# Optimization experiments

Measured on AMD Instinct MI355X. Metric: run time of the kernel, lower is better.

The kernel has to match this reference:

```python
import jax, jax.numpy as jnp
import numpy as np

V, K, H, B = 50000, 50, 300, 512
C_WEIGHTS = 0.0005
C_TOPICS = 5e-06
BN_EPS = 1e-5


def _bn(x, g, b, m, v):
    # eval-mode BatchNorm1d with running stats
    return (x - m) * jax.lax.rsqrt(v + BN_EPS) * g + b


def setup_inputs() -> dict:
    key = jax.random.key(0)
    ks = jax.random.split(key, 16)
    s = 0.02
    inp = {
        "bows": jax.random.uniform(ks[0], (B, V), jnp.float32),
        "normalized_bows": jax.random.uniform(ks[1], (B, V), jnp.float32),
        "labels": jax.random.normal(ks[2], (B,), jnp.float32),
        # encoder q_theta: Linear(V,H) -> relu -> BN -> Linear(H,H) -> relu -> BN
        "W1": jax.random.normal(ks[3], (H, V), jnp.float32) * s,
        "b1": jnp.zeros((H,), jnp.float32),
        "W2": jax.random.normal(ks[4], (H, H), jnp.float32) * s,
        "b2": jnp.zeros((H,), jnp.float32),
        "bn1_g": jnp.ones((H,), jnp.float32),
        "bn1_b": jnp.zeros((H,), jnp.float32),
        "bn1_m": jnp.zeros((H,), jnp.float32),
        "bn1_v": jnp.ones((H,), jnp.float32),
        "bn2_g": jnp.ones((H,), jnp.float32),
        "bn2_b": jnp.zeros((H,), jnp.float32),
        "bn2_m": jnp.zeros((H,), jnp.float32),
        "bn2_v": jnp.ones((H,), jnp.float32),
        "muW": jax.random.normal(ks[5], (K, H), jnp.float32) * s,
        "mub": jnp.zeros((K,), jnp.float32),
        "lsW": jax.random.normal(ks[6], (K, H), jnp.float32) * s,
        "lsb": jnp.zeros((K,), jnp.float32),
        "logit_betas": jax.random.normal(ks[7], (V, K), jnp.float32),
        "gammas": jax.random.normal(ks[8], (V, K), jnp.float32),
        "base_rates": jax.random.normal(ks[9], (V,), jnp.float32),
        "bow_w": jax.random.normal(ks[10], (V,), jnp.float32) * s,
        "bow_b": jnp.zeros((), jnp.float32),
        "topic_w": jax.random.normal(ks[11], (K,), jnp.float32) * s,
        "topic_b": jnp.zeros((), jnp.float32),
    }
    return inp


def reference(bows, normalized_bows, labels, W1, b1, W2, b2,
              bn1_g, bn1_b, bn1_m, bn1_v, bn2_g, bn2_b, bn2_m, bn2_v,
              muW, mub, lsW, lsb, logit_betas, gammas, base_rates,
              bow_w, bow_b, topic_w, topic_b):
    # ---- encode (eval mode: reparameterize returns mu) ----
    h = _bn(jax.nn.relu(normalized_bows @ W1.T + b1), bn1_g, bn1_b, bn1_m, bn1_v)
    h = _bn(jax.nn.relu(h @ W2.T + b2), bn2_g, bn2_b, bn2_m, bn2_v)
    mu = h @ muW.T + mub                       # [B, K]
    logsigma = h @ lsW.T + lsb                 # [B, K]
    kld_theta = -0.5 * jnp.mean(jnp.sum(1.0 + logsigma - mu ** 2 - jnp.exp(logsigma), axis=-1))
    theta = jax.nn.softmax(mu, axis=-1)        # [B, K]

    # ---- decode + reconstruction loss ----
    logits = theta @ logit_betas.T + base_rates          # [B, V]
    preds = jnp.log(jax.nn.softmax(logits, axis=-1) + 1e-06)
    recon_loss = -jnp.mean(jnp.sum(preds * bows, axis=1))

    # ---- other_loss: L1 on base_rates ----
    other_loss = C_WEIGHTS * jnp.sum(jnp.abs(base_rates))

    # ---- predict_labels (hstm-all), reordered contraction: (bows @ scaled_beta) * theta
    scaled_beta = logit_betas * gammas                   # [V, K]
    het_term = jnp.sum((normalized_bows @ scaled_beta) * theta, axis=1)  # == (bows * (theta @ scaled_beta.T)).sum(1)
    expected_pred = het_term + (normalized_bows @ bow_w + bow_b) + (theta @ topic_w + topic_b)

    other_loss = other_loss + jnp.mean((expected_pred - labels) ** 2)
    other_loss = other_loss + C_TOPICS * jnp.sum(jnp.abs(gammas))
    other_loss = other_loss + C_WEIGHTS * jnp.linalg.norm(bow_w)

    return recon_loss, other_loss, kld_theta
```

## Files before the change

kernel.cpp:

```cpp
#include <hip/hip_runtime.h>
#include <hip/hip_bf16.h>
#include <math.h>


#define B_  512
#define V_  50000
#define VP  50016
#define K_  50
#define H_  300
#define KP  64
#define NW  384
#define NSTEP 1563
#define NCVT 7327
#define NSB  782
#define NACV 12504

typedef __attribute__((ext_vector_type(8))) short short8;
typedef __attribute__((ext_vector_type(4))) float f32x4;

static __device__ __forceinline__ short bf16s(float f) {
  unsigned int u = __builtin_bit_cast(unsigned int, f);
  u += 0x7fffu + ((u >> 16) & 1u);
  return (short)(u >> 16);
}

static __device__ __forceinline__ unsigned int pkbf(float lo, float hi) {
  __hip_bfloat162 t = __float22bfloat162_rn(float2{lo, hi});
  unsigned int u; __builtin_memcpy(&u, &t, 4); return u;
}

static __device__ __forceinline__ short8 to_bf8(float4 a, float4 b) {
  unsigned int u[4];
  u[0] = pkbf(a.x, a.y); u[1] = pkbf(a.z, a.w);
  u[2] = pkbf(b.x, b.y); u[3] = pkbf(b.z, b.w);
  short8 r; __builtin_memcpy(&r, u, 16); return r;
}

__global__ __launch_bounds__(256) void k_prep(
    const float* __restrict__ W1,
    const float* __restrict__ beta, const float* __restrict__ gamma,
    const float* __restrict__ br,   const float* __restrict__ bw,
    const float* __restrict__ nb,
    short* __restrict__ Wcatb, short* __restrict__ betab,
    short* __restrict__ nbb,
    float* __restrict__ pg, float* __restrict__ pbr, float* __restrict__ pbw2)
{
  __shared__ short sbt[64 * 52];
  __shared__ short bbt[64 * 52];
  __shared__ float redA[4];
  const int tid = threadIdx.x;
  const short8 z8 = {0, 0, 0, 0, 0, 0, 0, 0};

  if (blockIdx.x < NCVT) {
    const int idx = blockIdx.x * 256 + tid;
    if (idx >= NSTEP * 300 * 4) return;
    const int st = idx / 1200;
    const int rem = idx - st * 1200;
    const int n = rem >> 2, kq = rem & 3;
    const int kbase = st * 32 + kq * 8;
    short8 o = z8;
    if (kbase + 8 <= V_) {
      const float4* p = (const float4*)(W1 + (size_t)n * V_ + kbase);
      o = to_bf8(p[0], p[1]);
    }
    *(short8*)(Wcatb + (size_t)st * 12288 + n * 32 + kq * 8) = o;
    return;
  }

  if (blockIdx.x >= NCVT + NSB) {
    const int idx = (blockIdx.x - (NCVT + NSB)) * 256 + tid;
    const int st = idx >> 11;
    const int r  = (idx >> 2) & 511;
    const int kq = idx & 3;
    const int kbase = st * 32 + kq * 8;
    short8 o = z8;
    if (kbase + 8 <= V_) {
      const float4* p = (const float4*)(nb + (size_t)r * V_ + kbase);
      o = to_bf8(p[0], p[1]);
    }
    *(short8*)(nbb + (size_t)st * 16384 + r * 32 + kq * 8) = o;
    return;
  }

  const int blk = blockIdx.x - NCVT;
  const int v0 = blk * 64;
  const int nvalid = (V_ - v0 < 64) ? (V_ - v0) : 64;
  const int nwrite = (VP - v0 < 64) ? (VP - v0) : 64;

  const int nf4 = (nvalid * 50) / 4;
  const float4* bsrc = (const float4*)(beta  + (size_t)v0 * 50);
  const float4* gsrc = (const float4*)(gamma + (size_t)v0 * 50);
  float gabs = 0.f;
  for (int f = tid; f < nf4; f += 256) {
    float4 bv = bsrc[f];
    float4 gv = gsrc[f];
    float be[4] = {bv.x, bv.y, bv.z, bv.w};
    float ge[4] = {gv.x, gv.y, gv.z, gv.w};
    #pragma unroll
    for (int e = 0; e < 4; ++e) {
      int idx = f * 4 + e;
      int j = idx / 50, k = idx - j * 50;
      gabs += fabsf(ge[e]);
      bbt[j * 52 + k] = bf16s(be[e]);
      sbt[j * 52 + k] = bf16s(be[e] * ge[e]);
    }
  }
  #pragma unroll
  for (int off = 1; off < 64; off <<= 1) gabs += __shfl_xor(gabs, off, 64);
  if ((tid & 63) == 0) redA[tid >> 6] = gabs;
  if (tid < 64) {
    float s1 = 0.f, s2 = 0.f;
    if (tid < nvalid) {
      s1 = fabsf(br[v0 + tid]);
      float w = bw[v0 + tid]; s2 = w * w;
    }
    #pragma unroll
    for (int off = 1; off < 64; off <<= 1) {
      s1 += __shfl_xor(s1, off, 64);
      s2 += __shfl_xor(s2, off, 64);
    }
    if (tid == 0) { pbr[blk] = s1; pbw2[blk] = s2; }
  }
  __syncthreads();
  if (tid == 0) pg[blk] = redA[0] + redA[1] + redA[2] + redA[3];

  const int j = tid & 63;
  const int q = tid >> 6;
  #pragma unroll
  for (int p = 0; p < 21; ++p) {
    const int kk = p * 4 + q;
    if (j < nwrite) {
      short val = 0;
      if (j < nvalid) {
        if (kk >= 20 && kk < 70)      val = sbt[j * 52 + (kk - 20)];
        else if (kk == 70)            val = bf16s(bw[v0 + j]);
      }
      Wcatb[(size_t)(blk * 2 + (j >> 5)) * 12288 + (300 + kk) * 32 + (j & 31)] = val;
    }
  }
  if (j < nvalid) {
    __attribute__((aligned(16))) short tmp[16];
    #pragma unroll
    for (int t = 0; t < 16; ++t) {
      int k = q * 16 + t;
      tmp[t] = (k < K_) ? bbt[j * 52 + k] : (short)0;
    }
    short8* dst = (short8*)(betab + (size_t)(v0 + j) * 64 + q * 16);
    dst[0] = *(const short8*)&tmp[0];
    dst[1] = *(const short8*)&tmp[8];
  }
}

__global__ __launch_bounds__(256, 3) void k_bg(
    const short* __restrict__ Ab, const short* __restrict__ Bb,
    float* __restrict__ part, int sps)
{
  const int t = blockIdx.x;
  const int s = t / 12;
  const int r = t % 12;
  const int bni = r % 3, bmi = r / 3;
  const int lane = threadIdx.x & 63, wv = threadIdx.x >> 6;
  const int l15 = lane & 15, quad = lane >> 4;
  const int m0 = bmi * 128 + (wv & 1) * 64;
  const int n0 = bni * 128 + (wv >> 1) * 64;
  int st0 = s * sps, st1 = st0 + sps;
  if (st0 > NSTEP) st0 = NSTEP;
  if (st1 > NSTEP) st1 = NSTEP;
  const int nst = st1 - st0;

  const short8* pa = (const short8*)Ab + (size_t)st0 * 2048 + (m0 + l15) * 4 + quad;
  const short8* pb = (const short8*)Bb + (size_t)st0 * 1536 + (n0 + l15) * 4 + quad;

  f32x4 acc[4][4];
  #pragma unroll
  for (int i = 0; i < 4; ++i)
    #pragma unroll
    for (int jj = 0; jj < 4; ++jj) acc[i][jj] = f32x4{0.f, 0.f, 0.f, 0.f};

  short8 A0[4], A1[4], B0[4], B1[4];

  auto ld = [&](short8 (&Af)[4], short8 (&Bf)[4]) {
    #pragma unroll
    for (int i = 0; i < 4; ++i) Af[i] = pa[i * 64];
    #pragma unroll
    for (int jj = 0; jj < 4; ++jj) Bf[jj] = pb[jj * 64];
    pa += 2048; pb += 1536;
  };
  auto comp = [&](short8 (&Af)[4], short8 (&Bf)[4]) {
    #pragma unroll
    for (int i = 0; i < 4; ++i)
      #pragma unroll
      for (int jj = 0; jj < 4; ++jj)
        acc[i][jj] = __builtin_amdgcn_mfma_f32_16x16x32_bf16(Af[i], Bf[jj], acc[i][jj], 0, 0, 0);
  };

  if (nst > 0) {
    ld(A0, B0);
    int k = 0;
    for (; k + 2 <= nst; k += 2) {
      ld(A1, B1);
      comp(A0, B0);
      if (k + 2 < nst) ld(A0, B0);
      comp(A1, B1);
    }
    if (k < nst) comp(A0, B0);
  }

  float* op = part + (size_t)s * (B_ * NW);
  #pragma unroll
  for (int i = 0; i < 4; ++i)
    #pragma unroll
    for (int jj = 0; jj < 4; ++jj)
      #pragma unroll
      for (int rr = 0; rr < 4; ++rr)
        op[(size_t)(m0 + 16 * i + quad * 4 + rr) * NW + (n0 + 16 * jj + l15)] = acc[i][jj][rr];
}

__global__ __launch_bounds__(320) void k_mlp(
    const float* __restrict__ part, int S,
    const float* __restrict__ b1,
    const float* __restrict__ g1, const float* __restrict__ bb1,
    const float* __restrict__ m1, const float* __restrict__ v1,
    const float* __restrict__ W2, const float* __restrict__ b2,
    const float* __restrict__ g2, const float* __restrict__ bb2,
    const float* __restrict__ m2, const float* __restrict__ v2,
    const float* __restrict__ muW, const float* __restrict__ mub,
    const float* __restrict__ lsW, const float* __restrict__ lsb,
    short* __restrict__ thetab, float* __restrict__ thetaf,
    float* __restrict__ hetmat, float* __restrict__ kldp)
{
  __shared__ __attribute__((aligned(16))) float h1s[H_];
  __shared__ __attribute__((aligned(16))) float h2s[H_];
  const int b = blockIdx.x;
  const int tid = threadIdx.x;
  const float* pb = part + (size_t)b * NW;

  if (tid < H_) {
    float s0 = 0.f, s1 = 0.f, s2 = 0.f, s3 = 0.f;
    int i = 0;
    for (; i + 4 <= S; i += 4) {
      s0 += pb[(size_t)(i + 0) * (B_ * NW) + tid];
      s1 += pb[(size_t)(i + 1) * (B_ * NW) + tid];
      s2 += pb[(size_t)(i + 2) * (B_ * NW) + tid];
      s3 += pb[(size_t)(i + 3) * (B_ * NW) + tid];
    }
    for (; i < S; ++i) s0 += pb[(size_t)i * (B_ * NW) + tid];
    float s = (s0 + s1) + (s2 + s3);
    float x = fmaxf(s + b1[tid], 0.f);
    h1s[tid] = (x - m1[tid]) * rsqrtf(v1[tid] + 1e-5f) * g1[tid] + bb1[tid];
  }
  if (tid < 51) {
    float s0 = 0.f, s1 = 0.f;
    int i = 0;
    for (; i + 2 <= S; i += 2) {
      s0 += pb[(size_t)(i + 0) * (B_ * NW) + 320 + tid];
      s1 += pb[(size_t)(i + 1) * (B_ * NW) + 320 + tid];
    }
    for (; i < S; ++i) s0 += pb[(size_t)i * (B_ * NW) + 320 + tid];
    hetmat[(size_t)b * KP + tid] = s0 + s1;
  }
  __syncthreads();
  if (tid < H_) {
    const float4* wr = (const float4*)(W2 + (size_t)tid * H_);
    const float4* hr = (const float4*)h1s;
    float acc = 0.f;
    for (int q = 0; q < H_ / 4; ++q) {
      float4 w = wr[q], h = hr[q];
      acc += w.x * h.x + w.y * h.y + w.z * h.z + w.w * h.w;
    }
    float x = fmaxf(acc + b2[tid], 0.f);
    h2s[tid] = (x - m2[tid]) * rsqrtf(v2[tid] + 1e-5f) * g2[tid] + bb2[tid];
  }
  __syncthreads();
  if (tid < 64) {
    float mu = 0.f, ls = 0.f;
    if (tid < K_) {
      const float4* mr = (const float4*)(muW + (size_t)tid * H_);
      const float4* lr = (const float4*)(lsW + (size_t)tid * H_);
      const float4* hr = (const float4*)h2s;
      for (int q = 0; q < H_ / 4; ++q) {
        float4 h = hr[q], a = mr[q], c = lr[q];
        mu += a.x * h.x + a.y * h.y + a.z * h.z + a.w * h.w;
        ls += c.x * h.x + c.y * h.y + c.z * h.z + c.w * h.w;
      }
      mu += mub[tid]; ls += lsb[tid];
    }
    float term = (tid < K_) ? (1.f + ls - mu * mu - __expf(ls)) : 0.f;
    float ts = term;
    #pragma unroll
    for (int off = 1; off < 64; off <<= 1) ts += __shfl_xor(ts, off, 64);
    if (tid == 0) kldp[b] = ts;
    float mv = (tid < K_) ? mu : -INFINITY;
    #pragma unroll
    for (int off = 1; off < 64; off <<= 1) mv = fmaxf(mv, __shfl_xor(mv, off, 64));
    float e = (tid < K_) ? __expf(mu - mv) : 0.f;
    float se = e;
    #pragma unroll
    for (int off = 1; off < 64; off <<= 1) se += __shfl_xor(se, off, 64);
    float tv = (tid < K_) ? (e / se) : 0.f;
    thetaf[(size_t)b * KP + tid] = tv;
    thetab[(size_t)b * KP + tid] = bf16s(tv);
  }
}

__global__ __launch_bounds__(256, 2) void k_c1(
    const short* __restrict__ thetab, const short* __restrict__ betab,
    const float* __restrict__ br, float* __restrict__ c1p)
{
  const int blk = blockIdx.x;
  const int bm = blk & 7, vs = blk >> 3;
  const int lane = threadIdx.x & 63, wv = threadIdx.x >> 6;
  const int l15 = lane & 15, quad = lane >> 4;
  const int b0 = bm * 64 + wv * 16;
  const short8* arow = (const short8*)(thetab + (size_t)(b0 + l15) * KP);
  const short8 a0 = arow[quad], a1 = arow[4 + quad];
  int t0 = vs * 33, t1 = t0 + 33; if (t1 > 3125) t1 = 3125;
  float p0 = 0.f, p1 = 0.f, p2 = 0.f, p3 = 0.f;
  auto body = [&](int tt) {
    const int v0 = tt * 16;
    const short8* brow = (const short8*)(betab + (size_t)(v0 + l15) * KP);
    short8 q0 = brow[quad], q1 = brow[4 + quad];
    f32x4 acc = {0.f, 0.f, 0.f, 0.f};
    acc = __builtin_amdgcn_mfma_f32_16x16x32_bf16(a0, q0, acc, 0, 0, 0);
    acc = __builtin_amdgcn_mfma_f32_16x16x32_bf16(a1, q1, acc, 0, 0, 0);
    const float brv = br[v0 + l15];
    p0 += __expf(acc[0] + brv);
    p1 += __expf(acc[1] + brv);
    p2 += __expf(acc[2] + brv);
    p3 += __expf(acc[3] + brv);
  };
  int tt = t0;
  for (; tt + 2 <= t1; tt += 2) { body(tt); body(tt + 1); }
  if (tt < t1) body(tt);
  #pragma unroll
  for (int off = 1; off < 16; off <<= 1) {
    p0 += __shfl_xor(p0, off, 16);
    p1 += __shfl_xor(p1, off, 16);
    p2 += __shfl_xor(p2, off, 16);
    p3 += __shfl_xor(p3, off, 16);
  }
  if (l15 == 0) {
    float* dst = c1p + (size_t)vs * B_ + b0 + quad * 4;
    dst[0] = p0; dst[1] = p1; dst[2] = p2; dst[3] = p3;
  }
}

static __device__ __forceinline__ float blockred512(float x, float* red) {
  #pragma unroll
  for (int off = 1; off < 64; off <<= 1) x += __shfl_xor(x, off, 64);
  if ((threadIdx.x & 63) == 0) red[threadIdx.x >> 6] = x;
  __syncthreads();
  float r = 0.f;
  if (threadIdx.x == 0)
    for (int i = 0; i < 8; ++i) r += red[i];
  __syncthreads();
  return r;
}

__global__ __launch_bounds__(512) void k_d1(
    const float* __restrict__ c1p, const float* __restrict__ kldp,
    const float* __restrict__ pg, const float* __restrict__ pbr,
    const float* __restrict__ pbw2,
    const float* __restrict__ hetmat, const float* __restrict__ thetaf,
    const float* __restrict__ labels, const float* __restrict__ topic_w,
    const float* __restrict__ topic_b, const float* __restrict__ bow_b,
    float* __restrict__ lseb, float* __restrict__ out)
{
  __shared__ float red[8];
  const int b = threadIdx.x;
  float se = 0.f;
  for (int i = 0; i < 96; ++i) se += c1p[(size_t)i * B_ + b];
  lseb[b] = __logf(se);
  float het = 0.f, tpc = 0.f;
  #pragma unroll
  for (int k = 0; k < K_; ++k) {
    float th = thetaf[(size_t)b * KP + k];
    het += th * hetmat[(size_t)b * KP + k];
    tpc += th * topic_w[k];
  }
  float ep = het + hetmat[(size_t)b * KP + 50] + bow_b[0] + tpc + topic_b[0];
  float d = ep - labels[b];
  float mse  = blockred512(d * d, red);
  float kl   = blockred512(kldp[b], red);
  float sg = 0.f, sr = 0.f, sw = 0.f;
  for (int i = b; i < NSB; i += 512) { sg += pg[i]; sr += pbr[i]; sw += pbw2[i]; }
  sg = blockred512(sg, red);
  sr = blockred512(sr, red);
  sw = blockred512(sw, red);
  if (b == 0) {
    out[1] = 0.0005f * sr + mse / (float)B_ + 5e-6f * sg + 0.0005f * sqrtf(sw);
    out[2] = -0.5f * kl / (float)B_;
  }
}

__global__ __launch_bounds__(256, 2) void k_c2(
    const short* __restrict__ thetab, const short* __restrict__ betab,
    const float* __restrict__ br, const float* __restrict__ lseb,
    const float* __restrict__ bows, float* __restrict__ c2p)
{
  __shared__ float red[4];
  const int blk = blockIdx.x;
  const int bm = blk & 7, vs = blk >> 3;
  const int lane = threadIdx.x & 63, wv = threadIdx.x >> 6;
  const int l15 = lane & 15, quad = lane >> 4;
  const int b0 = bm * 64 + wv * 16;
  const short8* arow = (const short8*)(thetab + (size_t)(b0 + l15) * KP);
  const short8 a0 = arow[quad], a1 = arow[4 + quad];
  float lse4[4]; const float* bro[4];
  #pragma unroll
  for (int rr = 0; rr < 4; ++rr) {
    lse4[rr] = lseb[b0 + quad * 4 + rr];
    bro[rr] = bows + (size_t)(b0 + quad * 4 + rr) * V_;
  }
  int t0 = vs * 33, t1 = t0 + 33; if (t1 > 3125) t1 = 3125;
  float p = 0.f;
  auto body = [&](int tt) {
    const int v0 = tt * 16;
    const int v = v0 + l15;
    const short8* brow = (const short8*)(betab + (size_t)v * KP);
    short8 q0 = brow[quad], q1 = brow[4 + quad];
    f32x4 acc = {0.f, 0.f, 0.f, 0.f};
    acc = __builtin_amdgcn_mfma_f32_16x16x32_bf16(a0, q0, acc, 0, 0, 0);
    acc = __builtin_amdgcn_mfma_f32_16x16x32_bf16(a1, q1, acc, 0, 0, 0);
    const float brv = br[v];
    #pragma unroll
    for (int rr = 0; rr < 4; ++rr) {
      float l = acc[rr] + brv - lse4[rr];
      float pr = __logf(__expf(l) + 1e-6f);
      p += pr * bro[rr][v];
    }
  };
  int tt = t0;
  for (; tt + 2 <= t1; tt += 2) { body(tt); body(tt + 1); }
  if (tt < t1) body(tt);
  #pragma unroll
  for (int off = 1; off < 64; off <<= 1) p += __shfl_xor(p, off, 64);
  if (lane == 0) red[wv] = p;
  __syncthreads();
  if (threadIdx.x == 0) c2p[blk] = red[0] + red[1] + red[2] + red[3];
}

__global__ __launch_bounds__(256) void k_d2(
    const float* __restrict__ c2p, float* __restrict__ out)
{
  __shared__ float red[4];
  float s = 0.f;
  for (int i = threadIdx.x; i < 768; i += 256) s += c2p[i];
  #pragma unroll
  for (int off = 1; off < 64; off <<= 1) s += __shfl_xor(s, off, 64);
  if ((threadIdx.x & 63) == 0) red[threadIdx.x >> 6] = s;
  __syncthreads();
  if (threadIdx.x == 0)
    out[0] = -(red[0] + red[1] + red[2] + red[3]) / (float)B_;
}

extern "C" void kernel_launch(void* const* d_in, const int* in_sizes, int n_in,
                              void* d_out, int out_size, void* d_ws, size_t ws_size,
                              hipStream_t stream)
{
  const float* bows    = (const float*)d_in[0];
  const float* nb      = (const float*)d_in[1];
  const float* labels  = (const float*)d_in[2];
  const float* W1      = (const float*)d_in[3];
  const float* b1      = (const float*)d_in[4];
  const float* W2      = (const float*)d_in[5];
  const float* b2      = (const float*)d_in[6];
  const float* bn1_g   = (const float*)d_in[7];
  const float* bn1_b   = (const float*)d_in[8];
  const float* bn1_m   = (const float*)d_in[9];
  const float* bn1_v   = (const float*)d_in[10];
  const float* bn2_g   = (const float*)d_in[11];
  const float* bn2_b   = (const float*)d_in[12];
  const float* bn2_m   = (const float*)d_in[13];
  const float* bn2_v   = (const float*)d_in[14];
  const float* muW     = (const float*)d_in[15];
  const float* mub     = (const float*)d_in[16];
  const float* lsW     = (const float*)d_in[17];
  const float* lsb     = (const float*)d_in[18];
  const float* beta    = (const float*)d_in[19];
  const float* gamma   = (const float*)d_in[20];
  const float* brates  = (const float*)d_in[21];
  const float* bow_w   = (const float*)d_in[22];
  const float* bow_b   = (const float*)d_in[23];
  const float* topic_w = (const float*)d_in[24];
  const float* topic_b = (const float*)d_in[25];
  float* out = (float*)d_out;

  char* ws = (char*)d_ws;
  size_t off = 0;
  auto take = [&](size_t bytes) { void* p = ws + off; off = (off + bytes + 255) & ~(size_t)255; return p; };

  short* Wcatb   = (short*)take((size_t)NSTEP * 12288 * 2);
  short* nbb     = (short*)take((size_t)NSTEP * 16384 * 2);
  short* betab   = (short*)take((size_t)V_ * 64 * 2);
  short* thetab  = (short*)take((size_t)B_ * KP * 2);
  float* thetaf  = (float*)take((size_t)B_ * KP * 4);
  float* hetmat  = (float*)take((size_t)B_ * KP * 4);
  float* kldp    = (float*)take((size_t)B_ * 4);
  float* c1p     = (float*)take((size_t)96 * B_ * 4);
  float* c2p     = (float*)take((size_t)768 * 4);
  float* lse_    = (float*)take((size_t)B_ * 4);
  float* pg      = (float*)take((size_t)NSB * 4);
  float* pbr     = (float*)take((size_t)NSB * 4);
  float* pbw2    = (float*)take((size_t)NSB * 4);
  float* part1   = (float*)(ws + off);
  size_t remain = (ws_size > off) ? (ws_size - off) : 0;
  int S = (int)(remain / ((size_t)B_ * NW * 4));
  if (S > 64) S = 64;
  if (S < 1)  S = 1;
  const int sps = (NSTEP + S - 1) / S;

  k_prep<<<NCVT + NSB + NACV, 256, 0, stream>>>(
      W1, beta, gamma, brates, bow_w, nb, Wcatb, betab, nbb, pg, pbr, pbw2);
  k_bg  <<<12 * S, 256, 0, stream>>>(nbb, Wcatb, part1, sps);
  k_mlp <<<B_, 320, 0, stream>>>(part1, S, b1, bn1_g, bn1_b, bn1_m, bn1_v,
                                 W2, b2, bn2_g, bn2_b, bn2_m, bn2_v,
                                 muW, mub, lsW, lsb, thetab, thetaf, hetmat, kldp);
  k_c1  <<<8 * 96, 256, 0, stream>>>(thetab, betab, brates, c1p);
  k_d1  <<<1, 512, 0, stream>>>(c1p, kldp, pg, pbr, pbw2, hetmat, thetaf,
                                labels, topic_w, topic_b, bow_b, lse_, out);
  k_c2  <<<8 * 96, 256, 0, stream>>>(thetab, betab, brates, lse_, bows, c2p);
  k_d2  <<<1, 256, 0, stream>>>(c2p, out);
}
```

Baseline: 478.8 us.

## Tile bf16 conversion of W1 and normalized_bows through LDS for coalesced access

```diff
diff --git a/kernel.cpp b/kernel.cpp
--- a/kernel.cpp
+++ b/kernel.cpp
@@ -11,9 +11,11 @@
 #define KP  64
 #define NW  384
 #define NSTEP 1563
-#define NCVT 7327
 #define NSB  782
-#define NACV 12504
+#define TS   8
+#define NT_ST 196
+#define NB_W1T (5*NT_ST)
+#define NB_NBT (8*NT_ST)
 
 typedef __attribute__((ext_vector_type(8))) short short8;
 typedef __attribute__((ext_vector_type(4))) float f32x4;
@@ -27,13 +29,6 @@
 static __device__ __forceinline__ unsigned int pkbf(float lo, float hi) {
   __hip_bfloat162 t = __float22bfloat162_rn(float2{lo, hi});
   unsigned int u; __builtin_memcpy(&u, &t, 4); return u;
-}
-
-static __device__ __forceinline__ short8 to_bf8(float4 a, float4 b) {
-  unsigned int u[4];
-  u[0] = pkbf(a.x, a.y); u[1] = pkbf(a.z, a.w);
-  u[2] = pkbf(b.x, b.y); u[3] = pkbf(b.z, b.w);
-  short8 r; __builtin_memcpy(&r, u, 16); return r;
 }
 
 __global__ __launch_bounds__(256) void k_prep(
@@ -45,44 +40,60 @@
     short* __restrict__ nbb,
     float* __restrict__ pg, float* __restrict__ pbr, float* __restrict__ pbw2)
 {
-  __shared__ short sbt[64 * 52];
-  __shared__ short bbt[64 * 52];
-  __shared__ float redA[4];
+  __shared__ __attribute__((aligned(16))) short lds[16384];
   const int tid = threadIdx.x;
-  const short8 z8 = {0, 0, 0, 0, 0, 0, 0, 0};
-
-  if (blockIdx.x < NCVT) {
-    const int idx = blockIdx.x * 256 + tid;
-    if (idx >= NSTEP * 300 * 4) return;
-    const int st = idx / 1200;
-    const int rem = idx - st * 1200;
-    const int n = rem >> 2, kq = rem & 3;
-    const int kbase = st * 32 + kq * 8;
-    short8 o = z8;
-    if (kbase + 8 <= V_) {
-      const float4* p = (const float4*)(W1 + (size_t)n * V_ + kbase);
-      o = to_bf8(p[0], p[1]);
-    }
-    *(short8*)(Wcatb + (size_t)st * 12288 + n * 32 + kq * 8) = o;
+
+  if (blockIdx.x < NB_W1T || blockIdx.x >= NB_W1T + NSB) {
+    const float* src; short* dst; int r0, nrows, frame, blk;
+    if (blockIdx.x < NB_W1T) {
+      blk = blockIdx.x; src = W1; dst = Wcatb; frame = 12288;
+      const int band = blk / NT_ST;
+      r0 = band * 64; nrows = (band == 4) ? 44 : 64;
+    } else {
+      blk = blockIdx.x - (NB_W1T + NSB); src = nb; dst = nbb; frame = 16384;
+      const int band = blk / NT_ST;
+      r0 = band * 64; nrows = 64;
+    }
+    const int stile = blk % NT_ST;
+    const int s0 = stile * TS;
+    int ns = NSTEP - s0; if (ns > TS) ns = TS;
+
+    const int row = tid >> 2, p = tid & 3;
+    if (row < nrows) {
+      const float4* rp = (const float4*)(src + (size_t)(r0 + row) * V_) + (size_t)s0 * 8;
+      const int c4lim = 12500 - s0 * 8;
+      auto doj = [&](int j) {
+        const int f4 = p + 4 * j;
+        float4 v = {0.f, 0.f, 0.f, 0.f};
+        if (f4 < c4lim) v = rp[f4];
+        unsigned int u0 = pkbf(v.x, v.y), u1 = pkbf(v.z, v.w);
+        unsigned long long uu = ((unsigned long long)u1 << 32) | (unsigned long long)u0;
+        *(unsigned long long*)((char*)lds + ((f4 >> 3) * 4096 + row * 64 + (f4 & 7) * 8)) = uu;
+      };
+      if (ns == TS) {
+        #pragma unroll
+        for (int jj = 0; jj < 8; ++jj) doj(jj);
+        #pragma unroll
+        for (int jj = 8; jj < 16; ++jj) doj(jj);
+      } else {
+        for (int j = 0; j < 2 * ns; ++j) doj(j);
+      }
+    }
+    __syncthreads();
+    for (int stl = 0; stl < ns; ++stl) {
+      short* db = dst + (size_t)(s0 + stl) * frame + r0 * 32;
+      const short8* sb = (const short8*)((char*)lds + stl * 4096);
+      for (int w = tid; w < nrows * 4; w += 256)
+        *(short8*)(db + w * 8) = sb[w];
+    }
     return;
   }
 
-  if (blockIdx.x >= NCVT + NSB) {
-    const int idx = (blockIdx.x - (NCVT + NSB)) * 256 + tid;
-    const int st = idx >> 11;
-    const int r  = (idx >> 2) & 511;
-    const int kq = idx & 3;
-    const int kbase = st * 32 + kq * 8;
-    short8 o = z8;
-    if (kbase + 8 <= V_) {
-      const float4* p = (const float4*)(nb + (size_t)r * V_ + kbase);
-      o = to_bf8(p[0], p[1]);
-    }
-    *(short8*)(nbb + (size_t)st * 16384 + r * 32 + kq * 8) = o;
-    return;
-  }
-
-  const int blk = blockIdx.x - NCVT;
+  short* sbt = lds;
+  short* bbt = lds + 64 * 52;
+  float* redA = (float*)(lds + 8192);
+
+  const int blk = blockIdx.x - NB_W1T;
   const int v0 = blk * 64;
   const int nvalid = (V_ - v0 < 64) ? (V_ - v0) : 64;
   const int nwrite = (VP - v0 < 64) ? (VP - v0) : 64;
@@ -510,7 +521,7 @@
   if (S < 1)  S = 1;
   const int sps = (NSTEP + S - 1) / S;
 
-  k_prep<<<NCVT + NSB + NACV, 256, 0, stream>>>(
+  k_prep<<<NB_W1T + NSB + NB_NBT, 256, 0, stream>>>(
       W1, beta, gamma, brates, bow_w, nb, Wcatb, betab, nbb, pg, pbr, pbw2);
   k_bg  <<<12 * S, 256, 0, stream>>>(nbb, Wcatb, part1, sps);
   k_mlp <<<B_, 320, 0, stream>>>(part1, S, b1, bn1_g, bn1_b, bn1_m, bn1_v,
```

Measured after the change: 478.5 us. Within noise of the previous version (-0.1%).

## Fuse fp32-to-bf16 conversion of W1 and normalized_bows into the GEMM loads

Applied to the files above, without the earlier changes.

```diff
diff --git a/kernel.cpp b/kernel.cpp
--- a/kernel.cpp
+++ b/kernel.cpp
@@ -11,9 +11,7 @@
 #define KP  64
 #define NW  384
 #define NSTEP 1563
-#define NCVT 7327
 #define NSB  782
-#define NACV 12504
 
 typedef __attribute__((ext_vector_type(8))) short short8;
 typedef __attribute__((ext_vector_type(4))) float f32x4;
@@ -36,53 +34,18 @@
   short8 r; __builtin_memcpy(&r, u, 16); return r;
 }
 
-__global__ __launch_bounds__(256) void k_prep(
-    const float* __restrict__ W1,
+__global__ __launch_bounds__(256) void k_prep_beta(
     const float* __restrict__ beta, const float* __restrict__ gamma,
     const float* __restrict__ br,   const float* __restrict__ bw,
-    const float* __restrict__ nb,
-    short* __restrict__ Wcatb, short* __restrict__ betab,
-    short* __restrict__ nbb,
+    short* __restrict__ bgcat, short* __restrict__ betab,
     float* __restrict__ pg, float* __restrict__ pbr, float* __restrict__ pbw2)
 {
   __shared__ short sbt[64 * 52];
   __shared__ short bbt[64 * 52];
   __shared__ float redA[4];
   const int tid = threadIdx.x;
-  const short8 z8 = {0, 0, 0, 0, 0, 0, 0, 0};
-
-  if (blockIdx.x < NCVT) {
-    const int idx = blockIdx.x * 256 + tid;
-    if (idx >= NSTEP * 300 * 4) return;
-    const int st = idx / 1200;
-    const int rem = idx - st * 1200;
-    const int n = rem >> 2, kq = rem & 3;
-    const int kbase = st * 32 + kq * 8;
-    short8 o = z8;
-    if (kbase + 8 <= V_) {
-      const float4* p = (const float4*)(W1 + (size_t)n * V_ + kbase);
-      o = to_bf8(p[0], p[1]);
-    }
-    *(short8*)(Wcatb + (size_t)st * 12288 + n * 32 + kq * 8) = o;
-    return;
-  }
-
-  if (blockIdx.x >= NCVT + NSB) {
-    const int idx = (blockIdx.x - (NCVT + NSB)) * 256 + tid;
-    const int st = idx >> 11;
-    const int r  = (idx >> 2) & 511;
-    const int kq = idx & 3;
-    const int kbase = st * 32 + kq * 8;
-    short8 o = z8;
-    if (kbase + 8 <= V_) {
-      const float4* p = (const float4*)(nb + (size_t)r * V_ + kbase);
-      o = to_bf8(p[0], p[1]);
-    }
-    *(short8*)(nbb + (size_t)st * 16384 + r * 32 + kq * 8) = o;
-    return;
-  }
-
-  const int blk = blockIdx.x - NCVT;
+
+  const int blk = blockIdx.x;
   const int v0 = blk * 64;
   const int nvalid = (V_ - v0 < 64) ? (V_ - v0) : 64;
   const int nwrite = (VP - v0 < 64) ? (VP - v0) : 64;
@@ -135,7 +98,7 @@
         if (kk >= 20 && kk < 70)      val = sbt[j * 52 + (kk - 20)];
         else if (kk == 70)            val = bf16s(bw[v0 + j]);
       }
-      Wcatb[(size_t)(blk * 2 + (j >> 5)) * 12288 + (300 + kk) * 32 + (j & 31)] = val;
+      bgcat[((size_t)(blk * 2 + (j >> 5)) * 84 + kk) * 32 + (j & 31)] = val;
     }
   }
   if (j < nvalid) {
@@ -152,12 +115,13 @@
 }
 
 __global__ __launch_bounds__(256, 3) void k_bg(
-    const short* __restrict__ Ab, const short* __restrict__ Bb,
+    const float* __restrict__ nb, const float* __restrict__ W1,
+    const short* __restrict__ bgcat,
     float* __restrict__ part, int sps)
 {
-  const int t = blockIdx.x;
-  const int s = t / 12;
-  const int r = t % 12;
+  const int S = gridDim.x / 12;
+  const int s = blockIdx.x % S;
+  const int r = blockIdx.x / S;
   const int bni = r % 3, bmi = r / 3;
   const int lane = threadIdx.x & 63, wv = threadIdx.x >> 6;
   const int l15 = lane & 15, quad = lane >> 4;
@@ -168,8 +132,7 @@
   if (st1 > NSTEP) st1 = NSTEP;
   const int nst = st1 - st0;
 
-  const short8* pa = (const short8*)Ab + (size_t)st0 * 2048 + (m0 + l15) * 4 + quad;
-  const short8* pb = (const short8*)Bb + (size_t)st0 * 1536 + (n0 + l15) * 4 + quad;
+  const short8 z8 = {0, 0, 0, 0, 0, 0, 0, 0};
 
   f32x4 acc[4][4];
   #pragma unroll
@@ -179,12 +142,28 @@
 
   short8 A0[4], A1[4], B0[4], B1[4];
 
-  auto ld = [&](short8 (&Af)[4], short8 (&Bf)[4]) {
-    #pragma unroll
-    for (int i = 0; i < 4; ++i) Af[i] = pa[i * 64];
-    #pragma unroll
-    for (int jj = 0; jj < 4; ++jj) Bf[jj] = pb[jj * 64];
-    pa += 2048; pb += 1536;
+  auto ld = [&](short8 (&Af)[4], short8 (&Bf)[4], int st) {
+    const int kb = st * 32 + quad * 8;
+    const bool ok = (kb + 8 <= V_);
+    #pragma unroll
+    for (int i = 0; i < 4; ++i) {
+      if (ok) {
+        const float4* p = (const float4*)(nb + (size_t)(m0 + l15 + 16 * i) * V_ + kb);
+        Af[i] = to_bf8(p[0], p[1]);
+      } else Af[i] = z8;
+    }
+    #pragma unroll
+    for (int jj = 0; jj < 4; ++jj) {
+      const int row = n0 + l15 + 16 * jj;
+      if (row < 300) {
+        if (ok) {
+          const float4* p = (const float4*)(W1 + (size_t)row * V_ + kb);
+          Bf[jj] = to_bf8(p[0], p[1]);
+        } else Bf[jj] = z8;
+      } else {
+        Bf[jj] = *(const short8*)(bgcat + ((size_t)st * 84 + (row - 300)) * 32 + quad * 8);
+      }
+    }
   };
   auto comp = [&](short8 (&Af)[4], short8 (&Bf)[4]) {
     #pragma unroll
@@ -195,12 +174,12 @@
   };
 
   if (nst > 0) {
-    ld(A0, B0);
+    ld(A0, B0, st0);
     int k = 0;
     for (; k + 2 <= nst; k += 2) {
-      ld(A1, B1);
+      ld(A1, B1, st0 + k + 1);
       comp(A0, B0);
-      if (k + 2 < nst) ld(A0, B0);
+      if (k + 2 < nst) ld(A0, B0, st0 + k + 2);
       comp(A1, B1);
     }
     if (k < nst) comp(A0, B0);
@@ -307,8 +286,7 @@
     const short* __restrict__ thetab, const short* __restrict__ betab,
     const float* __restrict__ br, float* __restrict__ c1p)
 {
-  const int blk = blockIdx.x;
-  const int bm = blk & 7, vs = blk >> 3;
+  const int bm = blockIdx.x / 96, vs = blockIdx.x % 96;
   const int lane = threadIdx.x & 63, wv = threadIdx.x >> 6;
   const int l15 = lane & 15, quad = lane >> 4;
   const int b0 = bm * 64 + wv * 16;
@@ -399,8 +377,7 @@
     const float* __restrict__ bows, float* __restrict__ c2p)
 {
   __shared__ float red[4];
-  const int blk = blockIdx.x;
-  const int bm = blk & 7, vs = blk >> 3;
+  const int bm = blockIdx.x / 96, vs = blockIdx.x % 96;
   const int lane = threadIdx.x & 63, wv = threadIdx.x >> 6;
   const int l15 = lane & 15, quad = lane >> 4;
   const int b0 = bm * 64 + wv * 16;
@@ -437,7 +414,7 @@
   for (int off = 1; off < 64; off <<= 1) p += __shfl_xor(p, off, 64);
   if (lane == 0) red[wv] = p;
   __syncthreads();
-  if (threadIdx.x == 0) c2p[blk] = red[0] + red[1] + red[2] + red[3];
+  if (threadIdx.x == 0) c2p[(size_t)vs * 8 + bm] = red[0] + red[1] + red[2] + red[3];
 }
 
 __global__ __launch_bounds__(256) void k_d2(
@@ -490,8 +467,7 @@
   size_t off = 0;
   auto take = [&](size_t bytes) { void* p = ws + off; off = (off + bytes + 255) & ~(size_t)255; return p; };
 
-  short* Wcatb   = (short*)take((size_t)NSTEP * 12288 * 2);
-  short* nbb     = (short*)take((size_t)NSTEP * 16384 * 2);
+  short* bgcat   = (short*)take((size_t)NSTEP * 84 * 32 * 2);
   short* betab   = (short*)take((size_t)V_ * 64 * 2);
   short* thetab  = (short*)take((size_t)B_ * KP * 2);
   float* thetaf  = (float*)take((size_t)B_ * KP * 4);
@@ -510,9 +486,9 @@
   if (S < 1)  S = 1;
   const int sps = (NSTEP + S - 1) / S;
 
-  k_prep<<<NCVT + NSB + NACV, 256, 0, stream>>>(
-      W1, beta, gamma, brates, bow_w, nb, Wcatb, betab, nbb, pg, pbr, pbw2);
-  k_bg  <<<12 * S, 256, 0, stream>>>(nbb, Wcatb, part1, sps);
+  k_prep_beta<<<NSB, 256, 0, stream>>>(beta, gamma, brates, bow_w,
+                                       bgcat, betab, pg, pbr, pbw2);
+  k_bg  <<<12 * S, 256, 0, stream>>>(nb, W1, bgcat, part1, sps);
   k_mlp <<<B_, 320, 0, stream>>>(part1, S, b1, bn1_g, bn1_b, bn1_m, bn1_v,
                                  W2, b2, bn2_g, bn2_b, bn2_m, bn2_v,
                                  muW, mub, lsW, lsb, thetab, thetaf, hetmat, kldp);
```

Result: slower. 505.1 us (+5.5%).
